# Kernel tuning notes

Measured on AMD Instinct MI355X. Metric: run time of the kernel, lower is better.

## Reference

```python
import jax, jax.numpy as jnp
import numpy as np

E, TOPK, D, F, FS = 16, 4, 2560, 1664, 3328
B, S = 1, 2048


def setup_inputs() -> dict:
    key = jax.random.key(0)
    ks = jax.random.split(key, 8)
    sc = lambda *sh: 1.0 / np.sqrt(sh[-2] if len(sh) > 1 else 1.0)
    return {
        "hidden_states": jax.random.normal(ks[0], (B, S, D), jnp.float32),
        "router_weight": jax.random.normal(ks[1], (E, D), jnp.float32) * (1.0 / np.sqrt(D)),
        "w_gate": jax.random.normal(ks[2], (E, D, F), jnp.float32) * (1.0 / np.sqrt(D)),
        "w_up": jax.random.normal(ks[3], (E, D, F), jnp.float32) * (1.0 / np.sqrt(D)),
        "w_down": jax.random.normal(ks[4], (E, F, D), jnp.float32) * (1.0 / np.sqrt(F)),
        "sw_gate": jax.random.normal(ks[5], (D, FS), jnp.float32) * (1.0 / np.sqrt(D)),
        "sw_up": jax.random.normal(ks[6], (D, FS), jnp.float32) * (1.0 / np.sqrt(D)),
        "sw_down": jax.random.normal(ks[7], (FS, D), jnp.float32) * (1.0 / np.sqrt(FS)),
    }


def reference(hidden_states, router_weight, w_gate, w_up, w_down, sw_gate, sw_up, sw_down):
    b, s, d = hidden_states.shape
    x = hidden_states.reshape(-1, d)  # [T, D]
    T = x.shape[0]

    # Router: linear -> softmax -> top-k -> renormalize (vLLM FusedMoE default)
    logits = x @ router_weight.T                      # [T, E]
    probs = jax.nn.softmax(logits, axis=-1)
    topk_w, topk_idx = jax.lax.top_k(probs, TOPK)     # [T, K]
    topk_w = topk_w / jnp.sum(topk_w, axis=-1, keepdims=True)
    combine = jnp.zeros((T, E), x.dtype).at[jnp.arange(T)[:, None], topk_idx].add(topk_w)  # [T, E]

    # Expert SiLU-gated MLPs (dense-dispatch reference for grouped GEMM)
    g = jnp.einsum('td,edf->tef', x, w_gate)          # [T, E, F]
    u = jnp.einsum('td,edf->tef', x, w_up)
    h = jax.nn.silu(g) * u
    y = jnp.einsum('tef,efd->ted', h, w_down)         # [T, E, D]
    sparse_out = jnp.einsum('ted,te->td', y, combine)

    # Shared expert: LlamaMLP with silu gate, no bias
    shared_out = (jax.nn.silu(x @ sw_gate) * (x @ sw_up)) @ sw_down

    return (sparse_out + shared_out).reshape(b, s, d)
```

## Files before the change

kernel.cpp:

```cpp
#include <hip/hip_runtime.h>
#include <hip/hip_bf16.h>
#include <stdint.h>

#define E_N 16
#define TOPK 4
#define DD 2560
#define FF 1664
#define FSS 3328
#define TT 2048

typedef __attribute__((ext_vector_type(8))) __bf16 bf16x8;
typedef __attribute__((ext_vector_type(4))) float f32x4;

__device__ __forceinline__ unsigned short f2bf(float f) {
  return __builtin_bit_cast(unsigned short, (__bf16)f);
}
__device__ __forceinline__ float bf2f(unsigned short u) {
  return __builtin_bit_cast(float, (unsigned int)u << 16);
}
__device__ __forceinline__ unsigned int pk2(float a, float b) {
  return (unsigned int)f2bf(a) | ((unsigned int)f2bf(b) << 16);
}

#define GLOAD16(g, l)                                                          \
  __builtin_amdgcn_global_load_lds(                                            \
      (const __attribute__((address_space(1))) void*)(g),                      \
      (__attribute__((address_space(3))) void*)(l), 16, 0, 0)

__device__ __forceinline__ void swz_block(int& bm, int& bn, int& bz) {
  int gx = gridDim.x, gy = gridDim.y;
  int nwg = gx * gy * gridDim.z;
  int flat = blockIdx.x + gx * (blockIdx.y + gy * blockIdx.z);
  if ((nwg & 7) == 0) flat = (flat & 7) * (nwg >> 3) + (flat >> 3);
  bm = flat % gx;
  int rest = flat / gx;
  bn = rest % gy;
  bz = rest / gy;
}

__global__ __launch_bounds__(256) void cvt_bf16_kernel(const float* __restrict__ in,
                                                       unsigned short* __restrict__ out) {
  size_t i = ((size_t)blockIdx.x * 256 + threadIdx.x) * 4;
  float4 v = *reinterpret_cast<const float4*>(in + i);
  ushort4 o;
  o.x = f2bf(v.x); o.y = f2bf(v.y); o.z = f2bf(v.z); o.w = f2bf(v.w);
  *reinterpret_cast<ushort4*>(out + i) = o;
}

__global__ __launch_bounds__(256) void tcvt_kernel(const float* __restrict__ in,
                                                   unsigned short* __restrict__ out,
                                                   int K, int N) {
  __shared__ float lds[64 * 65];
  int z = blockIdx.z;
  in += (size_t)z * K * N;
  out += (size_t)z * K * N;
  int k0 = blockIdx.x * 64, n0 = blockIdx.y * 64;
  int t = threadIdx.x;
#pragma unroll
  for (int j = 0; j < 4; ++j) {
    int idx = j * 256 + t;
    int r = idx >> 4, c = (idx & 15) * 4;
    float4 v = *reinterpret_cast<const float4*>(in + (size_t)(k0 + r) * N + n0 + c);
    lds[r * 65 + c] = v.x;
    lds[r * 65 + c + 1] = v.y;
    lds[r * 65 + c + 2] = v.z;
    lds[r * 65 + c + 3] = v.w;
  }
  __syncthreads();
#pragma unroll
  for (int j = 0; j < 2; ++j) {
    int idx = j * 256 + t;
    int n = idx >> 3, kg = (idx & 7) * 8;
    float a0 = lds[(kg + 0) * 65 + n], a1 = lds[(kg + 1) * 65 + n];
    float a2 = lds[(kg + 2) * 65 + n], a3 = lds[(kg + 3) * 65 + n];
    float a4 = lds[(kg + 4) * 65 + n], a5 = lds[(kg + 5) * 65 + n];
    float a6 = lds[(kg + 6) * 65 + n], a7 = lds[(kg + 7) * 65 + n];
    uint4 o{pk2(a0, a1), pk2(a2, a3), pk2(a4, a5), pk2(a6, a7)};
    *reinterpret_cast<uint4*>(out + (size_t)(n0 + n) * K + k0 + kg) = o;
  }
}

__global__ __launch_bounds__(256) void router_kernel(const float* __restrict__ x,
                                                     const float* __restrict__ rw,
                                                     int* __restrict__ cnt,
                                                     int* __restrict__ list,
                                                     float* __restrict__ tw) {
  int t = blockIdx.x;
  const float* xr = x + (size_t)t * DD;
  __shared__ float logits[E_N];
  int lane = threadIdx.x & 63, wid = threadIdx.x >> 6;
  for (int ee = 0; ee < 4; ++ee) {
    int e = wid * 4 + ee;
    const float* wr = rw + (size_t)e * DD;
    float p = 0.f;
    for (int d = lane; d < DD; d += 64) p += xr[d] * wr[d];
#pragma unroll
    for (int off = 32; off > 0; off >>= 1) p += __shfl_down(p, off);
    if (lane == 0) logits[e] = p;
  }
  __syncthreads();
  if (threadIdx.x == 0) {
    float mx = -1e30f;
    for (int e = 0; e < E_N; ++e) mx = fmaxf(mx, logits[e]);
    float pe[E_N];
    for (int e = 0; e < E_N; ++e) pe[e] = __expf(logits[e] - mx);
    int idx[TOPK]; float val[TOPK]; float s4 = 0.f;
    unsigned used = 0;
    for (int k = 0; k < TOPK; ++k) {
      int bi = 0; float bv = -1.f;
      for (int e = 0; e < E_N; ++e)
        if (!((used >> e) & 1) && pe[e] > bv) { bv = pe[e]; bi = e; }
      used |= 1u << bi; idx[k] = bi; val[k] = bv; s4 += bv;
    }
    float inv = 1.f / s4;
    for (int k = 0; k < TOPK; ++k) {
      int e2 = idx[k];
      int pos = atomicAdd(&cnt[e2], 1);
      list[e2 * TT + pos] = t * 4 + k;
      tw[t * 4 + k] = val[k] * inv;
    }
  }
}

template <int MODE, int SHIFT>
__device__ __forceinline__ void gemm_body(
    const unsigned short* __restrict__ A0, const unsigned short* __restrict__ W0,
    void* __restrict__ O0, const int* lst, const float* __restrict__ tw,
    int M, int Kt, int Nt, int m0, int n0) {
  __shared__ __align__(16) unsigned short ldsA[8192];
  __shared__ __align__(16) unsigned short ldsB[8192];

  int tid = threadIdx.x, lane = tid & 63, w = tid >> 6;

  const unsigned short* pA[4];
  const unsigned short* pB[4];
#pragma unroll
  for (int j = 0; j < 4; ++j) {
    int row = j * 32 + (tid >> 3);
    int cs = (tid & 7) ^ (row & 7);
    int ar = min(m0 + row, M - 1);
    int code = lst ? lst[ar] : ar;
    int arow = SHIFT ? (lst ? (code >> 2) : code) : code;
    pA[j] = A0 + (size_t)arow * Kt + cs * 8;
    pB[j] = W0 + (size_t)(n0 + j * 32 + (tid >> 3)) * Kt + cs * 8;
  }

  auto issue = [&](int kt) {
    int koff = kt * 64;
#pragma unroll
    for (int j = 0; j < 4; ++j) {
      GLOAD16(pA[j] + koff, ldsA + j * 2048 + tid * 8);
      GLOAD16(pB[j] + koff, ldsB + j * 2048 + tid * 8);
    }
  };

  int wr = (w >> 1) * 64, wc = (w & 1) * 64;
  int aoff[4][2], boff[4][2];
#pragma unroll
  for (int m = 0; m < 4; ++m) {
    int r = wr + m * 16 + (lane & 15);
    int rb = wc + m * 16 + (lane & 15);
#pragma unroll
    for (int kh = 0; kh < 2; ++kh) {
      int cg = kh * 4 + (lane >> 4);
      aoff[m][kh] = r * 64 + ((cg ^ (r & 7)) * 8);
      boff[m][kh] = rb * 64 + ((cg ^ (rb & 7)) * 8);
    }
  }

  f32x4 acc[4][4] = {};

  int nk = Kt / 64;
  issue(0);
  for (int kt = 0; kt < nk; ++kt) {
    __syncthreads();
#pragma unroll
    for (int kh = 0; kh < 2; ++kh) {
      bf16x8 a[4], b[4];
#pragma unroll
      for (int m = 0; m < 4; ++m)
        a[m] = __builtin_bit_cast(bf16x8, *reinterpret_cast<const uint4*>(ldsA + aoff[m][kh]));
#pragma unroll
      for (int n = 0; n < 4; ++n)
        b[n] = __builtin_bit_cast(bf16x8, *reinterpret_cast<const uint4*>(ldsB + boff[n][kh]));
      __builtin_amdgcn_s_setprio(1);
#pragma unroll
      for (int m = 0; m < 4; ++m)
#pragma unroll
        for (int n = 0; n < 4; ++n)
          acc[m][n] = __builtin_amdgcn_mfma_f32_16x16x32_bf16(a[m], b[n], acc[m][n], 0, 0, 0);
      __builtin_amdgcn_s_setprio(0);
    }
    __syncthreads();
    if (kt + 1 < nk) issue(kt + 1);
  }

#pragma unroll
  for (int m = 0; m < 4; ++m) {
#pragma unroll
    for (int q = 0; q < 4; ++q) {
      int lr = wr + m * 16 + (lane >> 4) * 4 + q;
      int grow = m0 + lr;
      if (grow < M) {
        int code = lst ? lst[grow] : grow;
        int col = n0 + wc + (lane & 15);
        if (MODE == 0) {
          unsigned short* Op = (unsigned short*)O0 + (size_t)code * Nt + col;
#pragma unroll
          for (int n = 0; n < 4; ++n) Op[n * 16] = f2bf(acc[m][n][q]);
        } else {
          float scale = tw ? tw[code] : 1.f;
          float* Op = (float*)O0 + (size_t)code * Nt + col;
#pragma unroll
          for (int n = 0; n < 4; ++n) Op[n * 16] = acc[m][n][q] * scale;
        }
      }
    }
  }
}

__global__ __launch_bounds__(256, 3) void gu2_kernel(
    const unsigned short* __restrict__ Xb,
    const unsigned short* __restrict__ WgT, const unsigned short* __restrict__ WuT,
    const unsigned short* __restrict__ SgT, const unsigned short* __restrict__ SuT,
    unsigned short* __restrict__ Gx, unsigned short* __restrict__ Ux,
    unsigned short* __restrict__ Gs, unsigned short* __restrict__ Us,
    const int* __restrict__ list, const int* __restrict__ cnt) {
  int bm, bn, z;
  swz_block(bm, bn, z);
  bool up = z >= 17;
  int ze = up ? z - 17 : z;
  const unsigned short* W0;
  unsigned short* O0;
  const int* lst = nullptr;
  int M, Nt;
  if (ze < E_N) {
    M = cnt[ze];
    lst = list + ze * TT;
    Nt = FF;
    W0 = (up ? WuT : WgT) + (size_t)ze * DD * FF;
    O0 = up ? Ux : Gx;
  } else {
    M = TT;
    Nt = FSS;
    W0 = up ? SuT : SgT;
    O0 = up ? Us : Gs;
  }
  int m0 = bm * 128, n0 = bn * 128;
  if (m0 >= M || n0 >= Nt) return;
  gemm_body<0, 1>(Xb, W0, O0, lst, nullptr, M, DD, Nt, m0, n0);
}

__global__ __launch_bounds__(256, 3) void dn2_kernel(
    const unsigned short* __restrict__ Hx, const unsigned short* __restrict__ Hs,
    const unsigned short* __restrict__ WdT, const unsigned short* __restrict__ SdT,
    float* __restrict__ Y, float* __restrict__ Ys,
    const int* __restrict__ list, const int* __restrict__ cnt,
    const float* __restrict__ tw) {
  int bm, bn, z;
  swz_block(bm, bn, z);
  const unsigned short* A0;
  const unsigned short* W0;
  float* O0;
  const int* lst = nullptr;
  const float* sc = nullptr;
  int M, Kt;
  if (z < E_N) {
    M = cnt[z];
    lst = list + z * TT;
    Kt = FF;
    A0 = Hx;
    W0 = WdT + (size_t)z * FF * DD;
    O0 = Y;
    sc = tw;
  } else {
    M = TT;
    Kt = FSS;
    A0 = Hs;
    W0 = SdT;
    O0 = Ys;
  }
  int m0 = bm * 128, n0 = bn * 128;
  if (m0 >= M) return;
  gemm_body<1, 0>(A0, W0, O0, lst, sc, M, Kt, DD, m0, n0);
}

__global__ __launch_bounds__(256) void h_kernel(const unsigned short* __restrict__ g,
                                                unsigned short* __restrict__ u) {
  size_t i = ((size_t)blockIdx.x * 256 + threadIdx.x) * 8;
  uint4 gv = *reinterpret_cast<const uint4*>(g + i);
  uint4 uv = *reinterpret_cast<const uint4*>(u + i);
  const unsigned int* gw = reinterpret_cast<const unsigned int*>(&gv);
  const unsigned int* uw = reinterpret_cast<const unsigned int*>(&uv);
  uint4 ov;
  unsigned int* ow = reinterpret_cast<unsigned int*>(&ov);
#pragma unroll
  for (int j = 0; j < 4; ++j) {
    float g0 = bf2f((unsigned short)(gw[j] & 0xffff));
    float g1 = bf2f((unsigned short)(gw[j] >> 16));
    float u0 = bf2f((unsigned short)(uw[j] & 0xffff));
    float u1 = bf2f((unsigned short)(uw[j] >> 16));
    float h0 = (g0 / (1.f + __expf(-g0))) * u0;
    float h1 = (g1 / (1.f + __expf(-g1))) * u1;
    ow[j] = pk2(h0, h1);
  }
  *reinterpret_cast<uint4*>(u + i) = ov;
}

__global__ __launch_bounds__(256) void combine_kernel(const float* __restrict__ Y,
                                                      const float* __restrict__ Ys,
                                                      float* __restrict__ out) {
  size_t i = ((size_t)blockIdx.x * 256 + threadIdx.x) * 4;
  size_t t = i / DD;
  int d = (int)(i % DD);
  float4 a = *reinterpret_cast<const float4*>(Ys + i);
#pragma unroll
  for (int k = 0; k < 4; ++k) {
    float4 v = *reinterpret_cast<const float4*>(Y + (t * 4 + k) * (size_t)DD + d);
    a.x += v.x; a.y += v.y; a.z += v.z; a.w += v.w;
  }
  *reinterpret_cast<float4*>(out + i) = a;
}

extern "C" void kernel_launch(void* const* d_in, const int* in_sizes, int n_in,
                              void* d_out, int out_size, void* d_ws, size_t ws_size,
                              hipStream_t stream) {
  const float* x  = (const float*)d_in[0];
  const float* rw = (const float*)d_in[1];
  const float* wg = (const float*)d_in[2];
  const float* wu = (const float*)d_in[3];
  const float* wd = (const float*)d_in[4];
  const float* sg = (const float*)d_in[5];
  const float* su = (const float*)d_in[6];
  const float* sd = (const float*)d_in[7];
  float* out = (float*)d_out;

  char* ws = (char*)d_ws;
  size_t off = 0;
  auto alloc = [&](size_t bytes) {
    off = (off + 255) & ~(size_t)255;
    void* p = ws + off;
    off += bytes;
    return p;
  };
  unsigned short* W1 = (unsigned short*)alloc((size_t)E_N * FF * DD * 2);
  unsigned short* W2 = (unsigned short*)alloc((size_t)E_N * FF * DD * 2);
  unsigned short* W3 = (unsigned short*)alloc((size_t)FSS * DD * 2);
  unsigned short* W4 = (unsigned short*)alloc((size_t)FSS * DD * 2);
  unsigned short* Xb = (unsigned short*)alloc((size_t)TT * DD * 2);
  unsigned short* Gx = (unsigned short*)alloc((size_t)4 * TT * FF * 2);
  unsigned short* Hx = (unsigned short*)alloc((size_t)4 * TT * FF * 2);
  unsigned short* Gs = (unsigned short*)alloc((size_t)TT * FSS * 2);
  unsigned short* Hs = (unsigned short*)alloc((size_t)TT * FSS * 2);
  float* Y  = (float*)alloc((size_t)4 * TT * DD * 4);
  float* Ys = (float*)alloc((size_t)TT * DD * 4);
  float* tw = (float*)alloc((size_t)4 * TT * 4);
  int* cnt  = (int*)alloc(E_N * 4);
  int* list = (int*)alloc((size_t)E_N * TT * 4);
  (void)ws_size; (void)in_sizes; (void)n_in; (void)out_size;

  hipMemsetAsync(cnt, 0, E_N * 4, stream);
  cvt_bf16_kernel<<<TT * DD / 4 / 256, 256, 0, stream>>>(x, Xb);
  router_kernel<<<TT, 256, 0, stream>>>(x, rw, cnt, list, tw);

  tcvt_kernel<<<dim3(DD / 64, FF / 64, E_N), 256, 0, stream>>>(wg, W1, DD, FF);
  tcvt_kernel<<<dim3(DD / 64, FF / 64, E_N), 256, 0, stream>>>(wu, W2, DD, FF);
  tcvt_kernel<<<dim3(DD / 64, FSS / 64, 1), 256, 0, stream>>>(sg, W3, DD, FSS);
  tcvt_kernel<<<dim3(DD / 64, FSS / 64, 1), 256, 0, stream>>>(su, W4, DD, FSS);

  gu2_kernel<<<dim3(TT / 128, FSS / 128, 34), 256, 0, stream>>>(
      Xb, W1, W2, W3, W4, Gx, Hx, Gs, Hs, list, cnt);

  h_kernel<<<(size_t)4 * TT * FF / 8 / 256, 256, 0, stream>>>(Gx, Hx);
  h_kernel<<<(size_t)TT * FSS / 8 / 256, 256, 0, stream>>>(Gs, Hs);

  tcvt_kernel<<<dim3(FF / 64, DD / 64, E_N), 256, 0, stream>>>(wd, W1, FF, DD);
  tcvt_kernel<<<dim3(FSS / 64, DD / 64, 1), 256, 0, stream>>>(sd, W2, FSS, DD);

  dn2_kernel<<<dim3(TT / 128, DD / 128, 17), 256, 0, stream>>>(
      Hx, Hs, W1, W2, Y, Ys, list, cnt, tw);

  combine_kernel<<<TT * DD / 4 / 256, 256, 0, stream>>>(Y, Ys, out);
}
```

Baseline: 1.195 ms.

## Switch MoE GEMMs to 256x256 tiles with 8 waves and double-buffered LDS pipeline

Replaces the 128x128, 4-wave GEMM body with a 256x256 tile computed by 8 waves, each owning a 128x64 sub-tile. The K step is split into four phases that prefetch the next K step into a second LDS buffer while MFMAs run on the current one, using explicit vmcnt waits and barriers. Tiles now extend past the N edge (1664 and 2560 are not multiples of 256), so B-row clamping and column guards are added. The aim is more data reuse per tile and hiding global-load latency. In exchange it uses 128 KB of LDS per block, gives fewer blocks for the small per-expert M, wastes work on partial tiles, and schedules many barriers.

```diff
diff --git a/kernel.cpp b/kernel.cpp
--- a/kernel.cpp
+++ b/kernel.cpp
@@ -26,6 +26,10 @@
   __builtin_amdgcn_global_load_lds(                                            \
       (const __attribute__((address_space(1))) void*)(g),                      \
       (__attribute__((address_space(3))) void*)(l), 16, 0, 0)
+
+#define SBAR() __builtin_amdgcn_s_barrier()
+#define SCHED0() __builtin_amdgcn_sched_barrier(0)
+#define VMW(N) asm volatile("s_waitcnt vmcnt(" #N ")" ::: "memory")
 
 __device__ __forceinline__ void swz_block(int& bm, int& bn, int& bz) {
   int gx = gridDim.x, gy = gridDim.y;
@@ -123,103 +127,132 @@
 }
 
 template <int MODE, int SHIFT>
-__device__ __forceinline__ void gemm_body(
+__device__ __forceinline__ void gemm8(
     const unsigned short* __restrict__ A0, const unsigned short* __restrict__ W0,
     void* __restrict__ O0, const int* lst, const float* __restrict__ tw,
     int M, int Kt, int Nt, int m0, int n0) {
-  __shared__ __align__(16) unsigned short ldsA[8192];
-  __shared__ __align__(16) unsigned short ldsB[8192];
+  __shared__ __align__(16) unsigned short lds[2][32768];
 
   int tid = threadIdx.x, lane = tid & 63, w = tid >> 6;
-
-  const unsigned short* pA[4];
-  const unsigned short* pB[4];
-#pragma unroll
-  for (int j = 0; j < 4; ++j) {
-    int row = j * 32 + (tid >> 3);
-    int cs = (tid & 7) ^ (row & 7);
+  int wm = w >> 2, wn = w & 3;
+
+  const unsigned short* pA[2];
+  const unsigned short* pB[2];
+  int ldso[2];
+#pragma unroll
+  for (int j = 0; j < 2; ++j) {
+    int cid = j * 512 + tid;
+    int row = cid >> 2, c = cid & 3;
+    int cs = c ^ ((row >> 1) & 3);
     int ar = min(m0 + row, M - 1);
     int code = lst ? lst[ar] : ar;
     int arow = SHIFT ? (lst ? (code >> 2) : code) : code;
     pA[j] = A0 + (size_t)arow * Kt + cs * 8;
-    pB[j] = W0 + (size_t)(n0 + j * 32 + (tid >> 3)) * Kt + cs * 8;
-  }
-
-  auto issue = [&](int kt) {
-    int koff = kt * 64;
-#pragma unroll
-    for (int j = 0; j < 4; ++j) {
-      GLOAD16(pA[j] + koff, ldsA + j * 2048 + tid * 8);
-      GLOAD16(pB[j] + koff, ldsB + j * 2048 + tid * 8);
+    int br = min(n0 + row, Nt - 1);
+    pB[j] = W0 + (size_t)br * Kt + cs * 8;
+    ldso[j] = cid * 8;
+  }
+
+  auto stage = [&](int kt, int s, int buf) {
+    int koff = kt * 64 + (s >> 1) * 32;
+    unsigned short* dst = &lds[buf][(s >> 1) * 8192 + ((s & 1) ? 16384 : 0)];
+    if (s & 1) {
+      GLOAD16(pB[0] + koff, dst + ldso[0]);
+      GLOAD16(pB[1] + koff, dst + ldso[1]);
+    } else {
+      GLOAD16(pA[0] + koff, dst + ldso[0]);
+      GLOAD16(pA[1] + koff, dst + ldso[1]);
     }
   };
 
-  int wr = (w >> 1) * 64, wc = (w & 1) * 64;
-  int aoff[4][2], boff[4][2];
-#pragma unroll
-  for (int m = 0; m < 4; ++m) {
-    int r = wr + m * 16 + (lane & 15);
-    int rb = wc + m * 16 + (lane & 15);
-#pragma unroll
-    for (int kh = 0; kh < 2; ++kh) {
-      int cg = kh * 4 + (lane >> 4);
-      aoff[m][kh] = r * 64 + ((cg ^ (r & 7)) * 8);
-      boff[m][kh] = rb * 64 + ((cg ^ (rb & 7)) * 8);
+  int cg = lane >> 4;
+  int aoff[8], boff[4];
+#pragma unroll
+  for (int mf = 0; mf < 8; ++mf) {
+    int r = wm * 128 + mf * 16 + (lane & 15);
+    aoff[mf] = r * 32 + ((cg ^ ((r >> 1) & 3)) * 8);
+  }
+#pragma unroll
+  for (int nf = 0; nf < 4; ++nf) {
+    int rb = wn * 64 + nf * 16 + (lane & 15);
+    boff[nf] = 16384 + rb * 32 + ((cg ^ ((rb >> 1) & 3)) * 8);
+  }
+
+  f32x4 acc[8][4] = {};
+  bf16x8 bfr[4];
+
+  int nk = Kt / 64;
+  stage(0, 0, 0); stage(0, 1, 0); stage(0, 2, 0); stage(0, 3, 0);
+  VMW(4); SCHED0();
+  SBAR(); SCHED0();
+
+  for (int kt = 0; kt < nk; ++kt) {
+    int buf = kt & 1;
+    const unsigned short* L = &lds[buf][0];
+    bool pf = (kt + 1 < nk);
+#pragma unroll
+    for (int ph = 0; ph < 4; ++ph) {
+      int ks = ph >> 1;
+      int mh = ph & 1;
+      bf16x8 afr[4];
+      if (mh == 0) {
+#pragma unroll
+        for (int nf = 0; nf < 4; ++nf)
+          bfr[nf] = __builtin_bit_cast(bf16x8,
+              *reinterpret_cast<const uint4*>(L + ks * 8192 + boff[nf]));
+      }
+#pragma unroll
+      for (int i = 0; i < 4; ++i)
+        afr[i] = __builtin_bit_cast(bf16x8,
+            *reinterpret_cast<const uint4*>(L + ks * 8192 + aoff[mh * 4 + i]));
+      if (pf) stage(kt + 1, ph, buf ^ 1);
+      if (ph == 1) {
+        if (pf) { VMW(4); } else { VMW(0); }
+      } else if (ph == 3 && pf) {
+        VMW(4);
+      }
+      SCHED0();
+      SBAR(); SCHED0();
+      __builtin_amdgcn_s_setprio(1);
+#pragma unroll
+      for (int i = 0; i < 4; ++i)
+#pragma unroll
+        for (int nf = 0; nf < 4; ++nf)
+          acc[mh * 4 + i][nf] =
+              __builtin_amdgcn_mfma_f32_16x16x32_bf16(afr[i], bfr[nf], acc[mh * 4 + i][nf], 0, 0, 0);
+      __builtin_amdgcn_s_setprio(0);
+      SCHED0();
+      SBAR(); SCHED0();
     }
   }
 
-  f32x4 acc[4][4] = {};
-
-  int nk = Kt / 64;
-  issue(0);
-  for (int kt = 0; kt < nk; ++kt) {
-    __syncthreads();
-#pragma unroll
-    for (int kh = 0; kh < 2; ++kh) {
-      bf16x8 a[4], b[4];
-#pragma unroll
-      for (int m = 0; m < 4; ++m)
-        a[m] = __builtin_bit_cast(bf16x8, *reinterpret_cast<const uint4*>(ldsA + aoff[m][kh]));
-#pragma unroll
-      for (int n = 0; n < 4; ++n)
-        b[n] = __builtin_bit_cast(bf16x8, *reinterpret_cast<const uint4*>(ldsB + boff[n][kh]));
-      __builtin_amdgcn_s_setprio(1);
-#pragma unroll
-      for (int m = 0; m < 4; ++m)
-#pragma unroll
-        for (int n = 0; n < 4; ++n)
-          acc[m][n] = __builtin_amdgcn_mfma_f32_16x16x32_bf16(a[m], b[n], acc[m][n], 0, 0, 0);
-      __builtin_amdgcn_s_setprio(0);
-    }
-    __syncthreads();
-    if (kt + 1 < nk) issue(kt + 1);
-  }
-
-#pragma unroll
-  for (int m = 0; m < 4; ++m) {
+#pragma unroll
+  for (int mf = 0; mf < 8; ++mf) {
 #pragma unroll
     for (int q = 0; q < 4; ++q) {
-      int lr = wr + m * 16 + (lane >> 4) * 4 + q;
+      int lr = wm * 128 + mf * 16 + (lane >> 4) * 4 + q;
       int grow = m0 + lr;
       if (grow < M) {
         int code = lst ? lst[grow] : grow;
-        int col = n0 + wc + (lane & 15);
+        int col = n0 + wn * 64 + (lane & 15);
         if (MODE == 0) {
           unsigned short* Op = (unsigned short*)O0 + (size_t)code * Nt + col;
 #pragma unroll
-          for (int n = 0; n < 4; ++n) Op[n * 16] = f2bf(acc[m][n][q]);
+          for (int nf = 0; nf < 4; ++nf)
+            if (col + nf * 16 < Nt) Op[nf * 16] = f2bf(acc[mf][nf][q]);
         } else {
           float scale = tw ? tw[code] : 1.f;
           float* Op = (float*)O0 + (size_t)code * Nt + col;
 #pragma unroll
-          for (int n = 0; n < 4; ++n) Op[n * 16] = acc[m][n][q] * scale;
+          for (int nf = 0; nf < 4; ++nf)
+            if (col + nf * 16 < Nt) Op[nf * 16] = acc[mf][nf][q] * scale;
         }
       }
     }
   }
 }
 
-__global__ __launch_bounds__(256, 3) void gu2_kernel(
+__global__ __launch_bounds__(512, 2) void gu8_kernel(
     const unsigned short* __restrict__ Xb,
     const unsigned short* __restrict__ WgT, const unsigned short* __restrict__ WuT,
     const unsigned short* __restrict__ SgT, const unsigned short* __restrict__ SuT,
@@ -246,12 +279,12 @@
     W0 = up ? SuT : SgT;
     O0 = up ? Us : Gs;
   }
-  int m0 = bm * 128, n0 = bn * 128;
+  int m0 = bm * 256, n0 = bn * 256;
   if (m0 >= M || n0 >= Nt) return;
-  gemm_body<0, 1>(Xb, W0, O0, lst, nullptr, M, DD, Nt, m0, n0);
-}
-
-__global__ __launch_bounds__(256, 3) void dn2_kernel(
+  gemm8<0, 1>(Xb, W0, O0, lst, nullptr, M, DD, Nt, m0, n0);
+}
+
+__global__ __launch_bounds__(512, 2) void dn8_kernel(
     const unsigned short* __restrict__ Hx, const unsigned short* __restrict__ Hs,
     const unsigned short* __restrict__ WdT, const unsigned short* __restrict__ SdT,
     float* __restrict__ Y, float* __restrict__ Ys,
@@ -280,9 +313,9 @@
     W0 = SdT;
     O0 = Ys;
   }
-  int m0 = bm * 128, n0 = bn * 128;
+  int m0 = bm * 256, n0 = bn * 256;
   if (m0 >= M) return;
-  gemm_body<1, 0>(A0, W0, O0, lst, sc, M, Kt, DD, m0, n0);
+  gemm8<1, 0>(A0, W0, O0, lst, sc, M, Kt, DD, m0, n0);
 }
 
 __global__ __launch_bounds__(256) void h_kernel(const unsigned short* __restrict__ g,
@@ -368,7 +401,7 @@
   tcvt_kernel<<<dim3(DD / 64, FSS / 64, 1), 256, 0, stream>>>(sg, W3, DD, FSS);
   tcvt_kernel<<<dim3(DD / 64, FSS / 64, 1), 256, 0, stream>>>(su, W4, DD, FSS);
 
-  gu2_kernel<<<dim3(TT / 128, FSS / 128, 34), 256, 0, stream>>>(
+  gu8_kernel<<<dim3(TT / 256, FSS / 256, 34), 512, 0, stream>>>(
       Xb, W1, W2, W3, W4, Gx, Hx, Gs, Hs, list, cnt);
 
   h_kernel<<<(size_t)4 * TT * FF / 8 / 256, 256, 0, stream>>>(Gx, Hx);
@@ -377,7 +410,7 @@
   tcvt_kernel<<<dim3(FF / 64, DD / 64, E_N), 256, 0, stream>>>(wd, W1, FF, DD);
   tcvt_kernel<<<dim3(FSS / 64, DD / 64, 1), 256, 0, stream>>>(sd, W2, FSS, DD);
 
-  dn2_kernel<<<dim3(TT / 128, DD / 128, 17), 256, 0, stream>>>(
+  dn8_kernel<<<dim3(TT / 256, DD / 256, 17), 512, 0, stream>>>(
       Hx, Hs, W1, W2, Y, Ys, list, cnt, tw);
 
   combine_kernel<<<TT * DD / 4 / 256, 256, 0, stream>>>(Y, Ys, out);
```

Result: slower. 1.283 ms (+7.4%).

## Fuse fp32 weight conversion into grouped GEMMs and fuse SiLU gating into gate/up

Applied to the files above, without the earlier changes.

Drops the separate transpose-and-convert passes over all expert and shared weights. The GEMMs now stream fp32 weights straight into LDS in their native [K,N] layout, converting to bf16 while gathering B fragments. The gate and up projections are computed in one kernel with two accumulator sets, and the SiLU*up product is applied in the epilogue, so the G buffer and the h_kernel pass are gone. In exchange each tile moves twice the weight bytes into LDS, does strided scalar LDS reads with per-element conversion, and the fused kernel uses more registers (launch bounds lowered to 2).

```diff
diff --git a/kernel.cpp b/kernel.cpp
--- a/kernel.cpp
+++ b/kernel.cpp
@@ -14,12 +14,6 @@
 
 __device__ __forceinline__ unsigned short f2bf(float f) {
   return __builtin_bit_cast(unsigned short, (__bf16)f);
-}
-__device__ __forceinline__ float bf2f(unsigned short u) {
-  return __builtin_bit_cast(float, (unsigned int)u << 16);
-}
-__device__ __forceinline__ unsigned int pk2(float a, float b) {
-  return (unsigned int)f2bf(a) | ((unsigned int)f2bf(b) << 16);
 }
 
 #define GLOAD16(g, l)                                                          \
@@ -45,39 +39,6 @@
   ushort4 o;
   o.x = f2bf(v.x); o.y = f2bf(v.y); o.z = f2bf(v.z); o.w = f2bf(v.w);
   *reinterpret_cast<ushort4*>(out + i) = o;
-}
-
-__global__ __launch_bounds__(256) void tcvt_kernel(const float* __restrict__ in,
-                                                   unsigned short* __restrict__ out,
-                                                   int K, int N) {
-  __shared__ float lds[64 * 65];
-  int z = blockIdx.z;
-  in += (size_t)z * K * N;
-  out += (size_t)z * K * N;
-  int k0 = blockIdx.x * 64, n0 = blockIdx.y * 64;
-  int t = threadIdx.x;
-#pragma unroll
-  for (int j = 0; j < 4; ++j) {
-    int idx = j * 256 + t;
-    int r = idx >> 4, c = (idx & 15) * 4;
-    float4 v = *reinterpret_cast<const float4*>(in + (size_t)(k0 + r) * N + n0 + c);
-    lds[r * 65 + c] = v.x;
-    lds[r * 65 + c + 1] = v.y;
-    lds[r * 65 + c + 2] = v.z;
-    lds[r * 65 + c + 3] = v.w;
-  }
-  __syncthreads();
-#pragma unroll
-  for (int j = 0; j < 2; ++j) {
-    int idx = j * 256 + t;
-    int n = idx >> 3, kg = (idx & 7) * 8;
-    float a0 = lds[(kg + 0) * 65 + n], a1 = lds[(kg + 1) * 65 + n];
-    float a2 = lds[(kg + 2) * 65 + n], a3 = lds[(kg + 3) * 65 + n];
-    float a4 = lds[(kg + 4) * 65 + n], a5 = lds[(kg + 5) * 65 + n];
-    float a6 = lds[(kg + 6) * 65 + n], a7 = lds[(kg + 7) * 65 + n];
-    uint4 o{pk2(a0, a1), pk2(a2, a3), pk2(a4, a5), pk2(a6, a7)};
-    *reinterpret_cast<uint4*>(out + (size_t)(n0 + n) * K + k0 + kg) = o;
-  }
 }
 
 __global__ __launch_bounds__(256) void router_kernel(const float* __restrict__ x,
@@ -122,73 +83,119 @@
   }
 }
 
-template <int MODE, int SHIFT>
-__device__ __forceinline__ void gemm_body(
-    const unsigned short* __restrict__ A0, const unsigned short* __restrict__ W0,
-    void* __restrict__ O0, const int* lst, const float* __restrict__ tw,
-    int M, int Kt, int Nt, int m0, int n0) {
+__global__ __launch_bounds__(256, 2) void guf_kernel(
+    const unsigned short* __restrict__ Xb,
+    const float* __restrict__ Wg, const float* __restrict__ Wu,
+    const float* __restrict__ Sg, const float* __restrict__ Su,
+    unsigned short* __restrict__ Hx, unsigned short* __restrict__ Hs,
+    const int* __restrict__ list, const int* __restrict__ cnt) {
+  int bm, bn, z;
+  swz_block(bm, bn, z);
+  const float *G0, *U0;
+  unsigned short* O0;
+  const int* lst = nullptr;
+  int M, Nt;
+  if (z < E_N) {
+    M = cnt[z]; lst = list + z * TT; Nt = FF;
+    G0 = Wg + (size_t)z * DD * FF; U0 = Wu + (size_t)z * DD * FF; O0 = Hx;
+  } else {
+    M = TT; Nt = FSS; G0 = Sg; U0 = Su; O0 = Hs;
+  }
+  int m0 = bm * 128, n0 = bn * 128;
+  if (m0 >= M || n0 >= Nt) return;
+
   __shared__ __align__(16) unsigned short ldsA[8192];
-  __shared__ __align__(16) unsigned short ldsB[8192];
+  __shared__ __align__(16) float ldsG[8192];
+  __shared__ __align__(16) float ldsU[8192];
 
   int tid = threadIdx.x, lane = tid & 63, w = tid >> 6;
 
   const unsigned short* pA[4];
-  const unsigned short* pB[4];
 #pragma unroll
   for (int j = 0; j < 4; ++j) {
-    int row = j * 32 + (tid >> 3);
-    int cs = (tid & 7) ^ (row & 7);
+    int q = j * 256 + tid;
+    int row = q >> 3, c = q & 7;
+    int cs = c ^ (row & 7);
     int ar = min(m0 + row, M - 1);
     int code = lst ? lst[ar] : ar;
-    int arow = SHIFT ? (lst ? (code >> 2) : code) : code;
-    pA[j] = A0 + (size_t)arow * Kt + cs * 8;
-    pB[j] = W0 + (size_t)(n0 + j * 32 + (tid >> 3)) * Kt + cs * 8;
+    int tok = lst ? (code >> 2) : code;
+    pA[j] = Xb + (size_t)tok * DD + cs * 8;
+  }
+  int offB[8];
+#pragma unroll
+  for (int j = 0; j < 8; ++j) {
+    int q = j * 256 + tid;
+    int k = q >> 5, cd = q & 31;
+    int cs = cd ^ (((k >> 3) & 1) << 2);
+    offB[j] = k * Nt + cs * 4;
   }
 
   auto issue = [&](int kt) {
-    int koff = kt * 64;
-#pragma unroll
-    for (int j = 0; j < 4; ++j) {
-      GLOAD16(pA[j] + koff, ldsA + j * 2048 + tid * 8);
-      GLOAD16(pB[j] + koff, ldsB + j * 2048 + tid * 8);
+    size_t ko = (size_t)kt * 64;
+#pragma unroll
+    for (int j = 0; j < 4; ++j)
+      GLOAD16(pA[j] + ko, ldsA + (j * 256 + tid) * 8);
+    const float* gb = G0 + n0 + ko * Nt;
+    const float* ub = U0 + n0 + ko * Nt;
+#pragma unroll
+    for (int j = 0; j < 8; ++j) {
+      GLOAD16(gb + offB[j], ldsG + (j * 256 + tid) * 4);
+      GLOAD16(ub + offB[j], ldsU + (j * 256 + tid) * 4);
     }
   };
 
   int wr = (w >> 1) * 64, wc = (w & 1) * 64;
-  int aoff[4][2], boff[4][2];
+  int aoff[4][2], bb[4][2];
 #pragma unroll
   for (int m = 0; m < 4; ++m) {
     int r = wr + m * 16 + (lane & 15);
-    int rb = wc + m * 16 + (lane & 15);
 #pragma unroll
     for (int kh = 0; kh < 2; ++kh) {
       int cg = kh * 4 + (lane >> 4);
       aoff[m][kh] = r * 64 + ((cg ^ (r & 7)) * 8);
-      boff[m][kh] = rb * 64 + ((cg ^ (rb & 7)) * 8);
-    }
-  }
-
-  f32x4 acc[4][4] = {};
-
-  int nk = Kt / 64;
+    }
+  }
+#pragma unroll
+  for (int nf = 0; nf < 4; ++nf) {
+    int nl = wc + nf * 16 + (lane & 15);
+#pragma unroll
+    for (int kh = 0; kh < 2; ++kh) {
+      int k0 = kh * 32 + (lane >> 4) * 8;
+      int f = ((lane >> 4) & 1) << 2;
+      bb[nf][kh] = k0 * 128 + ((((nl >> 2) & 31) ^ f) << 2) + (nl & 3);
+    }
+  }
+
+  f32x4 accG[4][4] = {};
+  f32x4 accU[4][4] = {};
+
+  int nk = DD / 64;
   issue(0);
   for (int kt = 0; kt < nk; ++kt) {
     __syncthreads();
 #pragma unroll
     for (int kh = 0; kh < 2; ++kh) {
-      bf16x8 a[4], b[4];
+      bf16x8 a[4], g[4], u[4];
 #pragma unroll
       for (int m = 0; m < 4; ++m)
         a[m] = __builtin_bit_cast(bf16x8, *reinterpret_cast<const uint4*>(ldsA + aoff[m][kh]));
 #pragma unroll
-      for (int n = 0; n < 4; ++n)
-        b[n] = __builtin_bit_cast(bf16x8, *reinterpret_cast<const uint4*>(ldsB + boff[n][kh]));
+      for (int nf = 0; nf < 4; ++nf) {
+        int b0 = bb[nf][kh];
+#pragma unroll
+        for (int j = 0; j < 8; ++j) {
+          g[nf][j] = (__bf16)ldsG[b0 + j * 128];
+          u[nf][j] = (__bf16)ldsU[b0 + j * 128];
+        }
+      }
       __builtin_amdgcn_s_setprio(1);
 #pragma unroll
       for (int m = 0; m < 4; ++m)
 #pragma unroll
-        for (int n = 0; n < 4; ++n)
-          acc[m][n] = __builtin_amdgcn_mfma_f32_16x16x32_bf16(a[m], b[n], acc[m][n], 0, 0, 0);
+        for (int nf = 0; nf < 4; ++nf) {
+          accG[m][nf] = __builtin_amdgcn_mfma_f32_16x16x32_bf16(a[m], g[nf], accG[m][nf], 0, 0, 0);
+          accU[m][nf] = __builtin_amdgcn_mfma_f32_16x16x32_bf16(a[m], u[nf], accU[m][nf], 0, 0, 0);
+        }
       __builtin_amdgcn_s_setprio(0);
     }
     __syncthreads();
@@ -203,108 +210,142 @@
       int grow = m0 + lr;
       if (grow < M) {
         int code = lst ? lst[grow] : grow;
-        int col = n0 + wc + (lane & 15);
-        if (MODE == 0) {
-          unsigned short* Op = (unsigned short*)O0 + (size_t)code * Nt + col;
-#pragma unroll
-          for (int n = 0; n < 4; ++n) Op[n * 16] = f2bf(acc[m][n][q]);
-        } else {
-          float scale = tw ? tw[code] : 1.f;
-          float* Op = (float*)O0 + (size_t)code * Nt + col;
-#pragma unroll
-          for (int n = 0; n < 4; ++n) Op[n * 16] = acc[m][n][q] * scale;
+        unsigned short* Hp = O0 + (size_t)code * Nt + n0 + wc + (lane & 15);
+#pragma unroll
+        for (int nf = 0; nf < 4; ++nf) {
+          float gg = accG[m][nf][q], uu = accU[m][nf][q];
+          Hp[nf * 16] = f2bf((gg / (1.f + __expf(-gg))) * uu);
         }
       }
     }
   }
 }
 
-__global__ __launch_bounds__(256, 3) void gu2_kernel(
-    const unsigned short* __restrict__ Xb,
-    const unsigned short* __restrict__ WgT, const unsigned short* __restrict__ WuT,
-    const unsigned short* __restrict__ SgT, const unsigned short* __restrict__ SuT,
-    unsigned short* __restrict__ Gx, unsigned short* __restrict__ Ux,
-    unsigned short* __restrict__ Gs, unsigned short* __restrict__ Us,
-    const int* __restrict__ list, const int* __restrict__ cnt) {
-  int bm, bn, z;
-  swz_block(bm, bn, z);
-  bool up = z >= 17;
-  int ze = up ? z - 17 : z;
-  const unsigned short* W0;
-  unsigned short* O0;
-  const int* lst = nullptr;
-  int M, Nt;
-  if (ze < E_N) {
-    M = cnt[ze];
-    lst = list + ze * TT;
-    Nt = FF;
-    W0 = (up ? WuT : WgT) + (size_t)ze * DD * FF;
-    O0 = up ? Ux : Gx;
-  } else {
-    M = TT;
-    Nt = FSS;
-    W0 = up ? SuT : SgT;
-    O0 = up ? Us : Gs;
-  }
-  int m0 = bm * 128, n0 = bn * 128;
-  if (m0 >= M || n0 >= Nt) return;
-  gemm_body<0, 1>(Xb, W0, O0, lst, nullptr, M, DD, Nt, m0, n0);
-}
-
-__global__ __launch_bounds__(256, 3) void dn2_kernel(
+__global__ __launch_bounds__(256, 3) void dnf_kernel(
     const unsigned short* __restrict__ Hx, const unsigned short* __restrict__ Hs,
-    const unsigned short* __restrict__ WdT, const unsigned short* __restrict__ SdT,
+    const float* __restrict__ Wd, const float* __restrict__ Sd,
     float* __restrict__ Y, float* __restrict__ Ys,
     const int* __restrict__ list, const int* __restrict__ cnt,
     const float* __restrict__ tw) {
   int bm, bn, z;
   swz_block(bm, bn, z);
   const unsigned short* A0;
-  const unsigned short* W0;
+  const float* B0;
   float* O0;
   const int* lst = nullptr;
   const float* sc = nullptr;
   int M, Kt;
   if (z < E_N) {
-    M = cnt[z];
-    lst = list + z * TT;
-    Kt = FF;
-    A0 = Hx;
-    W0 = WdT + (size_t)z * FF * DD;
-    O0 = Y;
-    sc = tw;
+    M = cnt[z]; lst = list + z * TT; Kt = FF;
+    A0 = Hx; B0 = Wd + (size_t)z * FF * DD; O0 = Y; sc = tw;
   } else {
-    M = TT;
-    Kt = FSS;
-    A0 = Hs;
-    W0 = SdT;
-    O0 = Ys;
+    M = TT; Kt = FSS; A0 = Hs; B0 = Sd; O0 = Ys;
   }
   int m0 = bm * 128, n0 = bn * 128;
   if (m0 >= M) return;
-  gemm_body<1, 0>(A0, W0, O0, lst, sc, M, Kt, DD, m0, n0);
-}
-
-__global__ __launch_bounds__(256) void h_kernel(const unsigned short* __restrict__ g,
-                                                unsigned short* __restrict__ u) {
-  size_t i = ((size_t)blockIdx.x * 256 + threadIdx.x) * 8;
-  uint4 gv = *reinterpret_cast<const uint4*>(g + i);
-  uint4 uv = *reinterpret_cast<const uint4*>(u + i);
-  const unsigned int* gw = reinterpret_cast<const unsigned int*>(&gv);
-  const unsigned int* uw = reinterpret_cast<const unsigned int*>(&uv);
-  uint4 ov;
-  unsigned int* ow = reinterpret_cast<unsigned int*>(&ov);
+
+  __shared__ __align__(16) unsigned short ldsA[8192];
+  __shared__ __align__(16) float ldsB[8192];
+
+  int tid = threadIdx.x, lane = tid & 63, w = tid >> 6;
+
+  const unsigned short* pA[4];
 #pragma unroll
   for (int j = 0; j < 4; ++j) {
-    float g0 = bf2f((unsigned short)(gw[j] & 0xffff));
-    float g1 = bf2f((unsigned short)(gw[j] >> 16));
-    float u0 = bf2f((unsigned short)(uw[j] & 0xffff));
-    float u1 = bf2f((unsigned short)(uw[j] >> 16));
-    float h0 = (g0 / (1.f + __expf(-g0))) * u0;
-    float h1 = (g1 / (1.f + __expf(-g1))) * u1;
-    ow[j] = pk2(h0, h1);
-  }
-  *reinterpret_cast<uint4*>(u + i) = ov;
+    int q = j * 256 + tid;
+    int row = q >> 3, c = q & 7;
+    int cs = c ^ (row & 7);
+    int ar = min(m0 + row, M - 1);
+    int code = lst ? lst[ar] : ar;
+    pA[j] = A0 + (size_t)code * Kt + cs * 8;
+  }
+  int offB[8];
+#pragma unroll
+  for (int j = 0; j < 8; ++j) {
+    int q = j * 256 + tid;
+    int k = q >> 5, cd = q & 31;
+    int cs = cd ^ (((k >> 3) & 1) << 2);
+    offB[j] = k * DD + cs * 4;
+  }
+
+  auto issue = [&](int kt) {
+    size_t ko = (size_t)kt * 64;
+#pragma unroll
+    for (int j = 0; j < 4; ++j)
+      GLOAD16(pA[j] + ko, ldsA + (j * 256 + tid) * 8);
+    const float* bbase = B0 + n0 + ko * DD;
+#pragma unroll
+    for (int j = 0; j < 8; ++j)
+      GLOAD16(bbase + offB[j], ldsB + (j * 256 + tid) * 4);
+  };
+
+  int wr = (w >> 1) * 64, wc = (w & 1) * 64;
+  int aoff[4][2], bb[4][2];
+#pragma unroll
+  for (int m = 0; m < 4; ++m) {
+    int r = wr + m * 16 + (lane & 15);
+#pragma unroll
+    for (int kh = 0; kh < 2; ++kh) {
+      int cg = kh * 4 + (lane >> 4);
+      aoff[m][kh] = r * 64 + ((cg ^ (r & 7)) * 8);
+    }
+  }
+#pragma unroll
+  for (int nf = 0; nf < 4; ++nf) {
+    int nl = wc + nf * 16 + (lane & 15);
+#pragma unroll
+    for (int kh = 0; kh < 2; ++kh) {
+      int k0 = kh * 32 + (lane >> 4) * 8;
+      int f = ((lane >> 4) & 1) << 2;
+      bb[nf][kh] = k0 * 128 + ((((nl >> 2) & 31) ^ f) << 2) + (nl & 3);
+    }
+  }
+
+  f32x4 acc[4][4] = {};
+
+  int nk = Kt / 64;
+  issue(0);
+  for (int kt = 0; kt < nk; ++kt) {
+    __syncthreads();
+#pragma unroll
+    for (int kh = 0; kh < 2; ++kh) {
+      bf16x8 a[4], b[4];
+#pragma unroll
+      for (int m = 0; m < 4; ++m)
+        a[m] = __builtin_bit_cast(bf16x8, *reinterpret_cast<const uint4*>(ldsA + aoff[m][kh]));
+#pragma unroll
+      for (int nf = 0; nf < 4; ++nf) {
+        int b0 = bb[nf][kh];
+#pragma unroll
+        for (int j = 0; j < 8; ++j) b[nf][j] = (__bf16)ldsB[b0 + j * 128];
+      }
+      __builtin_amdgcn_s_setprio(1);
+#pragma unroll
+      for (int m = 0; m < 4; ++m)
+#pragma unroll
+        for (int nf = 0; nf < 4; ++nf)
+          acc[m][nf] = __builtin_amdgcn_mfma_f32_16x16x32_bf16(a[m], b[nf], acc[m][nf], 0, 0, 0);
+      __builtin_amdgcn_s_setprio(0);
+    }
+    __syncthreads();
+    if (kt + 1 < nk) issue(kt + 1);
+  }
+
+#pragma unroll
+  for (int m = 0; m < 4; ++m) {
+#pragma unroll
+    for (int q = 0; q < 4; ++q) {
+      int lr = wr + m * 16 + (lane >> 4) * 4 + q;
+      int grow = m0 + lr;
+      if (grow < M) {
+        int code = lst ? lst[grow] : grow;
+        float scale = sc ? sc[code] : 1.f;
+        float* Op = O0 + (size_t)code * DD + n0 + wc + (lane & 15);
+#pragma unroll
+        for (int nf = 0; nf < 4; ++nf) Op[nf * 16] = acc[m][nf][q] * scale;
+      }
+    }
+  }
 }
 
 __global__ __launch_bounds__(256) void combine_kernel(const float* __restrict__ Y,
@@ -343,14 +384,8 @@
     off += bytes;
     return p;
   };
-  unsigned short* W1 = (unsigned short*)alloc((size_t)E_N * FF * DD * 2);
-  unsigned short* W2 = (unsigned short*)alloc((size_t)E_N * FF * DD * 2);
-  unsigned short* W3 = (unsigned short*)alloc((size_t)FSS * DD * 2);
-  unsigned short* W4 = (unsigned short*)alloc((size_t)FSS * DD * 2);
   unsigned short* Xb = (unsigned short*)alloc((size_t)TT * DD * 2);
-  unsigned short* Gx = (unsigned short*)alloc((size_t)4 * TT * FF * 2);
   unsigned short* Hx = (unsigned short*)alloc((size_t)4 * TT * FF * 2);
-  unsigned short* Gs = (unsigned short*)alloc((size_t)TT * FSS * 2);
   unsigned short* Hs = (unsigned short*)alloc((size_t)TT * FSS * 2);
   float* Y  = (float*)alloc((size_t)4 * TT * DD * 4);
   float* Ys = (float*)alloc((size_t)TT * DD * 4);
@@ -363,22 +398,11 @@
   cvt_bf16_kernel<<<TT * DD / 4 / 256, 256, 0, stream>>>(x, Xb);
   router_kernel<<<TT, 256, 0, stream>>>(x, rw, cnt, list, tw);
 
-  tcvt_kernel<<<dim3(DD / 64, FF / 64, E_N), 256, 0, stream>>>(wg, W1, DD, FF);
-  tcvt_kernel<<<dim3(DD / 64, FF / 64, E_N), 256, 0, stream>>>(wu, W2, DD, FF);
-  tcvt_kernel<<<dim3(DD / 64, FSS / 64, 1), 256, 0, stream>>>(sg, W3, DD, FSS);
-  tcvt_kernel<<<dim3(DD / 64, FSS / 64, 1), 256, 0, stream>>>(su, W4, DD, FSS);
-
-  gu2_kernel<<<dim3(TT / 128, FSS / 128, 34), 256, 0, stream>>>(
-      Xb, W1, W2, W3, W4, Gx, Hx, Gs, Hs, list, cnt);
-
-  h_kernel<<<(size_t)4 * TT * FF / 8 / 256, 256, 0, stream>>>(Gx, Hx);
-  h_kernel<<<(size_t)TT * FSS / 8 / 256, 256, 0, stream>>>(Gs, Hs);
-
-  tcvt_kernel<<<dim3(FF / 64, DD / 64, E_N), 256, 0, stream>>>(wd, W1, FF, DD);
-  tcvt_kernel<<<dim3(FSS / 64, DD / 64, 1), 256, 0, stream>>>(sd, W2, FSS, DD);
-
-  dn2_kernel<<<dim3(TT / 128, DD / 128, 17), 256, 0, stream>>>(
-      Hx, Hs, W1, W2, Y, Ys, list, cnt, tw);
+  guf_kernel<<<dim3(TT / 128, FSS / 128, E_N + 1), 256, 0, stream>>>(
+      Xb, wg, wu, sg, su, Hx, Hs, list, cnt);
+
+  dnf_kernel<<<dim3(TT / 128, DD / 128, E_N + 1), 256, 0, stream>>>(
+      Hx, Hs, wd, sd, Y, Ys, list, cnt, tw);
 
   combine_kernel<<<TT * DD / 4 / 256, 256, 0, stream>>>(Y, Ys, out);
 }
```

Result: slower. 3.350 ms (+180.4%).
